# Performance work log

Hardware: AMD Instinct MI355X
Metric: run time of the kernel (lower is better)

Reference implementation:

```python
import jax, jax.numpy as jnp
import numpy as np

N = 100000      # num nodes
E = 1600000     # num edges (before self-loops)
F_IN = 500      # num_features
H1, C1 = 8, 8   # heads, hidden_dim (layer 1, concat)
H2, C2 = 1, 16  # output_heads, num_classes (layer 2, mean)
NEG_SLOPE = 0.2


def setup_inputs() -> dict:
    key = jax.random.key(0)
    ks = jax.random.split(key, 10)
    x = jax.random.normal(ks[0], (N, F_IN), dtype=jnp.float32)
    edge_index = jax.random.randint(ks[1], (2, E), 0, N, dtype=jnp.int64)
    s = 0.05
    W1 = jax.random.normal(ks[2], (F_IN, H1 * C1), dtype=jnp.float32) * s
    a_src1 = jax.random.normal(ks[3], (H1, C1), dtype=jnp.float32) * s
    a_dst1 = jax.random.normal(ks[4], (H1, C1), dtype=jnp.float32) * s
    b1 = jnp.zeros((H1 * C1,), dtype=jnp.float32)
    W2 = jax.random.normal(ks[5], (H1 * C1, H2 * C2), dtype=jnp.float32) * s
    a_src2 = jax.random.normal(ks[6], (H2, C2), dtype=jnp.float32) * s
    a_dst2 = jax.random.normal(ks[7], (H2, C2), dtype=jnp.float32) * s
    b2 = jnp.zeros((C2,), dtype=jnp.float32)
    return {"x": x, "edge_index": edge_index, "W1": W1, "a_src1": a_src1,
            "a_dst1": a_dst1, "b1": b1, "W2": W2, "a_src2": a_src2,
            "a_dst2": a_dst2, "b2": b2}


def _gat_conv(x, src, dst, W, a_src, a_dst, bias, heads, out_c, concat):
    n = x.shape[0]
    xw = (x @ W).reshape(n, heads, out_c)                      # [N,H,C]
    # per-node attention halves, gathered per edge -> logits [E,H]
    s_src = jnp.einsum('nhc,hc->nh', xw, a_src)
    s_dst = jnp.einsum('nhc,hc->nh', xw, a_dst)
    e = s_src[src] + s_dst[dst]
    e = jnp.where(e > 0, e, NEG_SLOPE * e)                     # leaky_relu
    # segment softmax over incoming edges of each target node
    m = jax.ops.segment_max(e, dst, num_segments=n)            # [N,H]
    m = jnp.where(jnp.isfinite(m), m, 0.0)
    p = jnp.exp(e - m[dst])                                    # [E,H]
    denom = jax.ops.segment_sum(p, dst, num_segments=n)        # [N,H]
    alpha = p / denom[dst]                                     # [E,H]
    # scatter-aggregate weighted messages
    out = jax.ops.segment_sum(alpha[:, :, None] * xw[src], dst,
                              num_segments=n)                  # [N,H,C]
    if concat:
        out = out.reshape(n, heads * out_c)
    else:
        out = out.mean(axis=1)
    return out + bias


def reference(x, edge_index, W1, a_src1, a_dst1, b1, W2, a_src2, a_dst2, b2):
    # PyG GATConv adds self-loops by default
    loops = jnp.arange(N, dtype=edge_index.dtype)
    src = jnp.concatenate([edge_index[0], loops])
    dst = jnp.concatenate([edge_index[1], loops])
    # eval mode: dropout is identity
    h = _gat_conv(x, src, dst, W1, a_src1, a_dst1, b1, H1, C1, True)
    h = jax.nn.elu(h)
    h = _gat_conv(h, src, dst, W2, a_src2, a_dst2, b2, H2, C2, False)
    return jax.nn.log_softmax(h, axis=1)
```

## Files before the change

kernel.cpp:

```cpp
#include <hip/hip_runtime.h>
#include <hip/hip_bf16.h>
#include <math.h>

#define NEGS 0.2f
#define BSH 9
#define TS 4096

typedef __attribute__((ext_vector_type(8))) short bf16x8;
typedef __attribute__((ext_vector_type(8))) unsigned short u16x8;
typedef __attribute__((ext_vector_type(4))) float f32x4;

__device__ __forceinline__ unsigned short f2bf(float f) {
  __hip_bfloat16 h = __float2bfloat16(f);
  unsigned short u;
  __builtin_memcpy(&u, &h, 2);
  return u;
}
__device__ __forceinline__ float bf2f(unsigned short u) {
  return __uint_as_float((unsigned)u << 16);
}
__device__ __forceinline__ unsigned packbf(float lo, float hi) {
  return (unsigned)f2bf(lo) | ((unsigned)f2bf(hi) << 16);
}


__device__ __forceinline__ void dev_wcvt(const float* __restrict__ W1,
                                         unsigned short* __restrict__ Wb,
                                         int K, int Kp, int blk) {
  int t = blk * 256 + threadIdx.x;
  if (t >= Kp * 64) return;
  int kg = t >> 6, c = t & 63;
  float f = (kg < K) ? W1[(size_t)kg * 64 + c] : 0.f;
  size_t off = ((size_t)((kg >> 5) * 4 + ((kg >> 3) & 3)) * 512) + c * 8 + (kg & 7);
  Wb[off] = f2bf(f);
}

__device__ __forceinline__ void dev_thist(const int* __restrict__ ei,
                                          int* __restrict__ hist,
                                          int E, int NB, int tile) {
  __shared__ int lh[256];
  const int t = threadIdx.x;
  lh[t] = 0;
  __syncthreads();
  const int e0 = tile * TS;
#pragma unroll
  for (int j = 0; j < TS / 256; ++j) {
    int e = e0 + j * 256 + t;
    if (e < E) atomicAdd(&lh[ei[E + e] >> BSH], 1);
  }
  __syncthreads();
  if (t < NB) hist[tile * NB + t] = lh[t];
}

__device__ __forceinline__ void dev_bscan1(const int* __restrict__ hist,
                                           int* __restrict__ off_rel,
                                           int* __restrict__ total,
                                           int NT, int NB, int b) {
  __shared__ int sh[256];
  const int t = threadIdx.x;
  int t0 = 2 * t, t1 = 2 * t + 1;
  int v0 = (t0 < NT) ? hist[t0 * NB + b] : 0;
  int v1 = (t1 < NT) ? hist[t1 * NB + b] : 0;
  int ps = v0 + v1;
  sh[t] = ps;
  __syncthreads();
  for (int off = 1; off < 256; off <<= 1) {
    int v = (t >= off) ? sh[t - off] : 0;
    __syncthreads();
    sh[t] += v;
    __syncthreads();
  }
  int excl = sh[t] - ps;
  if (t0 < NT) off_rel[t0 * NB + b] = excl;
  if (t1 < NT) off_rel[t1 * NB + b] = excl + v0;
  if (t == 255) total[b] = sh[255];
}

__device__ __forceinline__ void dev_pscatter(const int* __restrict__ ei,
                                             const int* __restrict__ off_rel,
                                             const int* __restrict__ total,
                                             unsigned* __restrict__ pairs,
                                             int E, int NB, int tile) {
  __shared__ int cur[256];
  __shared__ int sb[256];
  const int t = threadIdx.x;
  int v = (t < NB) ? total[t] : 0;
  sb[t] = v;
  __syncthreads();
  for (int off = 1; off < 256; off <<= 1) {
    int x = (t >= off) ? sb[t - off] : 0;
    __syncthreads();
    sb[t] += x;
    __syncthreads();
  }
  if (t < NB) cur[t] = (sb[t] - v) + off_rel[tile * NB + t];
  __syncthreads();
  const int e0 = tile * TS;
#pragma unroll
  for (int j = 0; j < TS / 256; ++j) {
    int e = e0 + j * 256 + t;
    if (e < E) {
      int s = ei[e], d = ei[E + e];
      int pos = atomicAdd(&cur[d >> BSH], 1);
      pairs[pos] = ((unsigned)(d & ((1 << BSH) - 1)) << 23) | (unsigned)s;
    }
  }
}

__device__ __forceinline__ void dev_bcsr(const unsigned* __restrict__ pairs,
                                         const int* __restrict__ total,
                                         int* __restrict__ rowptr,
                                         int* __restrict__ col,
                                         int Nn, int E, int NB, int b) {
  __shared__ int cnt[1 << BSH];
  __shared__ int cu[1 << BSH];
  __shared__ int sh[256];
  __shared__ int P0, P1;
  const int t = threadIdx.x;
  const int d0 = b << BSH;
  const int dn = min(1 << BSH, Nn - d0);
  {
    int v = (t < NB) ? total[t] : 0;
    sh[t] = v;
    __syncthreads();
    for (int off = 1; off < 256; off <<= 1) {
      int x = (t >= off) ? sh[t - off] : 0;
      __syncthreads();
      sh[t] += x;
      __syncthreads();
    }
    if (t == b) { P0 = sh[t] - v; P1 = sh[t]; }
    __syncthreads();
  }
  const int p0 = P0, p1 = P1;
  const int rpb = p0 + d0;
  cnt[2 * t] = (2 * t < dn) ? 1 : 0;
  cnt[2 * t + 1] = (2 * t + 1 < dn) ? 1 : 0;
  __syncthreads();
  for (int i = p0 + t; i < p1; i += 256) atomicAdd(&cnt[pairs[i] >> 23], 1);
  __syncthreads();
  int a0 = cnt[2 * t], a1 = cnt[2 * t + 1];
  int ps = a0 + a1;
  sh[t] = ps;
  __syncthreads();
  for (int off = 1; off < 256; off <<= 1) {
    int v = (t >= off) ? sh[t - off] : 0;
    __syncthreads();
    sh[t] += v;
    __syncthreads();
  }
  int excl = sh[t] - ps;
#pragma unroll
  for (int u = 0; u < 2; ++u) {
    int i = 2 * t + u;
    int ex = (u == 0) ? excl : excl + a0;
    if (i < dn) {
      rowptr[d0 + i] = rpb + ex;
      col[rpb + ex] = d0 + i;
      cu[i] = ex + 1;
    }
  }
  if (b == NB - 1 && t == 0) rowptr[Nn] = E + Nn;
  __syncthreads();
  for (int i = p0 + t; i < p1; i += 256) {
    unsigned p = pairs[i];
    int pos = atomicAdd(&cu[p >> 23], 1);
    col[rpb + pos] = (int)(p & 0x7fffffu);
  }
}

__device__ __forceinline__ void dev_gemm(const float* __restrict__ A,
                                         const unsigned short* __restrict__ Wb,
                                         unsigned short* __restrict__ C,
                                         const float* __restrict__ a1s,
                                         const float* __restrict__ a1d,
                                         float* __restrict__ ssrc,
                                         float* __restrict__ sdst,
                                         int M, int K, int nck, int rowblk) {
  const int tid = threadIdx.x;
  const int lane = tid & 63;
  const int w = tid >> 6;
  const int r15 = lane & 15;
  const int kgrp = lane >> 4;
  const int bm = rowblk * 64;
  const int row = bm + w * 16 + r15;
  const float* Ar = A + (size_t)(row < M ? row : (M - 1)) * K;

  f32x4 acc[4] = {};

  for (int ck = 0; ck < nck; ++ck) {
#pragma unroll
    for (int ks = 0; ks < 2; ++ks) {
      const int k0 = ck * 64 + ks * 32 + kgrp * 8;
      bf16x8 af;
      if (ck < nck - 1) {
        const float4* g = (const float4*)(Ar + k0);
        float4 f0 = g[0], f1 = g[1];
        unsigned pk[4] = { packbf(f0.x, f0.y), packbf(f0.z, f0.w),
                           packbf(f1.x, f1.y), packbf(f1.z, f1.w) };
        af = *(bf16x8*)pk;
      } else {
        float f[8];
#pragma unroll
        for (int j = 0; j < 8; ++j) {
          int kk = k0 + j;
          f[j] = (kk < K) ? Ar[kk] : 0.f;
        }
        unsigned pk[4];
#pragma unroll
        for (int j = 0; j < 4; ++j) pk[j] = packbf(f[2 * j], f[2 * j + 1]);
        af = *(bf16x8*)pk;
      }
      const unsigned short* bb =
          Wb + ((size_t)((ck * 2 + ks) * 4 + kgrp) * 512) + r15 * 8;
      bf16x8 bf4[4];
#pragma unroll
      for (int nc = 0; nc < 4; ++nc)
        bf4[nc] = *(const bf16x8*)(bb + nc * 128);
#pragma unroll
      for (int nc = 0; nc < 4; ++nc)
        acc[nc] = __builtin_amdgcn_mfma_f32_16x16x32_bf16(af, bf4[nc], acc[nc], 0, 0, 0);
    }
  }
  float av[4], dv[4];
#pragma unroll
  for (int nc = 0; nc < 4; ++nc) {
    av[nc] = a1s[nc * 16 + r15];
    dv[nc] = a1d[nc * 16 + r15];
  }
#pragma unroll
  for (int j = 0; j < 4; ++j) {
    int grow = bm + w * 16 + kgrp * 4 + j;
    bool liv = grow < M;
#pragma unroll
    for (int nc = 0; nc < 4; ++nc) {
      if (liv) C[(size_t)grow * 64 + nc * 16 + r15] = f2bf(acc[nc][j]);
      float ss = acc[nc][j] * av[nc];
      float sd = acc[nc][j] * dv[nc];
      ss += __shfl_xor(ss, 1); ss += __shfl_xor(ss, 2); ss += __shfl_xor(ss, 4);
      sd += __shfl_xor(sd, 1); sd += __shfl_xor(sd, 2); sd += __shfl_xor(sd, 4);
      if ((r15 & 7) == 0 && liv) {
        int h = nc * 2 + (r15 >> 3);
        ssrc[grow * 8 + h] = ss;
        sdst[grow * 8 + h] = sd;
      }
    }
  }
}

__global__ __launch_bounds__(256) void k_A(const float* __restrict__ W1,
                                           unsigned short* __restrict__ Wb,
                                           int K, int Kp,
                                           const int* __restrict__ ei,
                                           int* __restrict__ hist,
                                           int E, int NB, int WCB) {
  int b = blockIdx.x;
  if (b < WCB) dev_wcvt(W1, Wb, K, Kp, b);
  else dev_thist(ei, hist, E, NB, b - WCB);
}

__global__ __launch_bounds__(256) void k_B1(const int* __restrict__ hist,
                                            int* __restrict__ off_rel,
                                            int* __restrict__ total,
                                            int NT, int NB,
                                            const float* __restrict__ A,
                                            const unsigned short* __restrict__ Wb,
                                            unsigned short* __restrict__ C,
                                            const float* __restrict__ a1s,
                                            const float* __restrict__ a1d,
                                            float* __restrict__ ssrc,
                                            float* __restrict__ sdst,
                                            int M, int K, int nck, int R0) {
  int b = blockIdx.x;
  if (b < NB) dev_bscan1(hist, off_rel, total, NT, NB, b);
  else dev_gemm(A, Wb, C, a1s, a1d, ssrc, sdst, M, K, nck, b - NB + R0);
}

__global__ __launch_bounds__(256) void k_B2(const int* __restrict__ ei,
                                            const int* __restrict__ off_rel,
                                            const int* __restrict__ total,
                                            unsigned* __restrict__ pairs,
                                            int E, int NB, int NT,
                                            const float* __restrict__ A,
                                            const unsigned short* __restrict__ Wb,
                                            unsigned short* __restrict__ C,
                                            const float* __restrict__ a1s,
                                            const float* __restrict__ a1d,
                                            float* __restrict__ ssrc,
                                            float* __restrict__ sdst,
                                            int M, int K, int nck, int R0) {
  int b = blockIdx.x;
  if (b < NT) dev_pscatter(ei, off_rel, total, pairs, E, NB, b);
  else dev_gemm(A, Wb, C, a1s, a1d, ssrc, sdst, M, K, nck, b - NT + R0);
}

__global__ __launch_bounds__(256) void k_B3(const unsigned* __restrict__ pairs,
                                            const int* __restrict__ total,
                                            int* __restrict__ rowptr,
                                            int* __restrict__ col,
                                            int Nn, int E, int NB,
                                            const float* __restrict__ A,
                                            const unsigned short* __restrict__ Wb,
                                            unsigned short* __restrict__ C,
                                            const float* __restrict__ a1s,
                                            const float* __restrict__ a1d,
                                            float* __restrict__ ssrc,
                                            float* __restrict__ sdst,
                                            int M, int K, int nck, int R0) {
  int b = blockIdx.x;
  if (b < NB) dev_bcsr(pairs, total, rowptr, col, Nn, E, NB, b);
  else dev_gemm(A, Wb, C, a1s, a1d, ssrc, sdst, M, K, nck, b - NB + R0);
}

__global__ __launch_bounds__(256) void k_agg1(const int* __restrict__ rowptr,
                                              const int* __restrict__ col,
                                              const float* __restrict__ ssrc,
                                              const float* __restrict__ sdst,
                                              const unsigned short* __restrict__ xwb,
                                              const float* __restrict__ b1,
                                              float* __restrict__ h1, int Nn) {
  int wid = (blockIdx.x * 256 + threadIdx.x) >> 6;
  if (wid >= Nn) return;
  int lane = threadIdx.x & 63;
  int slot = lane >> 3;
  int chg = lane & 7;
  float sd = sdst[wid * 8 + chg];
  int start = rowptr[wid], end = rowptr[wid + 1];
  float den = 0.f;
  float acc[8] = {};
  for (int it = start; it < end; it += 8) {
    int idx = it + slot;
    bool ok = idx < end;
    int s = col[ok ? idx : start];
    u16x8 pv = *(const u16x8*)(xwb + (size_t)s * 64 + chg * 8);
    float v = ssrc[s * 8 + chg] + sd;
    v = v > 0.f ? v : NEGS * v;
    float p = ok ? __expf(v) : 0.f;
    den += p;
#pragma unroll
    for (int j = 0; j < 8; ++j) acc[j] = fmaf(p, bf2f(pv[j]), acc[j]);
  }
#pragma unroll
  for (int off = 8; off < 64; off <<= 1) {
    den += __shfl_xor(den, off);
#pragma unroll
    for (int j = 0; j < 8; ++j) acc[j] += __shfl_xor(acc[j], off);
  }
  if (slot == 0) {
    float inv = 1.f / den;
    float o[8];
#pragma unroll
    for (int j = 0; j < 8; ++j) {
      float v = acc[j] * inv + b1[chg * 8 + j];
      o[j] = v > 0.f ? v : (__expf(v) - 1.f);
    }
    float* dst = h1 + (size_t)wid * 64 + chg * 8;
#pragma unroll
    for (int j = 0; j < 8; ++j) dst[j] = o[j];
  }
}

__global__ __launch_bounds__(256) void k_gemm2p(const float* __restrict__ h1,
                                                const float* __restrict__ W2,
                                                const float* __restrict__ asr,
                                                const float* __restrict__ adt,
                                                unsigned short* __restrict__ xw2b,
                                                float* __restrict__ ssrc,
                                                float* __restrict__ sdst, int Nn) {
  __shared__ float w[64 * 16];
  int tid = threadIdx.x;
  for (int i = tid; i < 1024; i += 256) w[i] = W2[i];
  __syncthreads();
  int idx = blockIdx.x * 256 + tid;
  if (idx >= Nn * 16) return;
  int n = idx >> 4, c = idx & 15;
  const float* hr = h1 + (size_t)n * 64;
  float acc = 0.f;
#pragma unroll 8
  for (int k = 0; k < 64; ++k) acc += hr[k] * w[k * 16 + c];
  xw2b[idx] = f2bf(acc);
  float ssv = acc * asr[c], sdv = acc * adt[c];
#pragma unroll
  for (int off = 1; off < 16; off <<= 1) {
    ssv += __shfl_xor(ssv, off);
    sdv += __shfl_xor(sdv, off);
  }
  if (c == 0) { ssrc[n] = ssv; sdst[n] = sdv; }
}

__global__ __launch_bounds__(256) void k_agg2(const int* __restrict__ rowptr,
                                              const int* __restrict__ col,
                                              const float* __restrict__ ssrc,
                                              const float* __restrict__ sdst,
                                              const unsigned short* __restrict__ xw2b,
                                              const float* __restrict__ b2,
                                              float* __restrict__ out, int Nn) {
  int wid = (blockIdx.x * 256 + threadIdx.x) >> 6;
  if (wid >= Nn) return;
  int lane = threadIdx.x & 63;
  int slot = lane >> 4, c = lane & 15;
  float sd = sdst[wid];
  int start = rowptr[wid], end = rowptr[wid + 1];
  float den = 0.f, acc = 0.f;
  int i = start + slot;
  for (; i + 4 < end; i += 8) {
    int s0 = col[i], s1 = col[i + 4];
    float w0 = bf2f(xw2b[(size_t)s0 * 16 + c]);
    float w1 = bf2f(xw2b[(size_t)s1 * 16 + c]);
    float v0 = ssrc[s0] + sd; v0 = v0 > 0.f ? v0 : NEGS * v0;
    float v1 = ssrc[s1] + sd; v1 = v1 > 0.f ? v1 : NEGS * v1;
    float p0 = __expf(v0), p1 = __expf(v1);
    den += p0 + p1;
    acc = fmaf(p0, w0, acc);
    acc = fmaf(p1, w1, acc);
  }
  if (i < end) {
    int s = col[i];
    float v = ssrc[s] + sd;
    v = v > 0.f ? v : NEGS * v;
    float p = __expf(v);
    den += p;
    acc = fmaf(p, bf2f(xw2b[(size_t)s * 16 + c]), acc);
  }
  den += __shfl_xor(den, 16);
  den += __shfl_xor(den, 32);
  acc += __shfl_xor(acc, 16);
  acc += __shfl_xor(acc, 32);
  float o = acc / den + b2[c];
  float mx = o;
#pragma unroll
  for (int off = 1; off < 16; off <<= 1) mx = fmaxf(mx, __shfl_xor(mx, off));
  float ex = __expf(o - mx);
  float ssum = ex;
#pragma unroll
  for (int off = 1; off < 16; off <<= 1) ssum += __shfl_xor(ssum, off);
  float r = o - mx - __logf(ssum);
  if (slot == 0) out[(size_t)wid * 16 + c] = r;
}

extern "C" void kernel_launch(void* const* d_in, const int* in_sizes, int n_in,
                              void* d_out, int out_size, void* d_ws, size_t ws_size,
                              hipStream_t stream) {
  const float* x      = (const float*)d_in[0];
  const int* ei       = (const int*)d_in[1];
  const float* W1     = (const float*)d_in[2];
  const float* a_src1 = (const float*)d_in[3];
  const float* a_dst1 = (const float*)d_in[4];
  const float* b1     = (const float*)d_in[5];
  const float* W2     = (const float*)d_in[6];
  const float* a_src2 = (const float*)d_in[7];
  const float* a_dst2 = (const float*)d_in[8];
  const float* b2     = (const float*)d_in[9];

  const int F    = in_sizes[2] / 64;
  const int Nn   = in_sizes[0] / F;
  const int E    = in_sizes[1] / 2;
  const int Etot = E + Nn;
  const int nck  = (F + 63) >> 6;
  const int Kp   = nck * 64;
  const int NB   = (Nn + (1 << BSH) - 1) >> BSH;
  const int NT   = (E + TS - 1) / TS;
  const int WCB  = (Kp * 64 + 255) / 256;
  const int GB   = (Nn + 63) / 64;
  const int G1   = (GB + 2) / 3;
  const int G2   = G1;
  const int G3   = GB - G1 - G2;

  float* ws = (float*)d_ws;
  unsigned short* xwb = (unsigned short*)ws;
  float* h1     = ws + (size_t)Nn * 32;
  float* ssrc1  = h1 + (size_t)Nn * 64;
  float* sdst1  = ssrc1 + (size_t)Nn * 8;
  int* rowptr   = (int*)(sdst1 + (size_t)Nn * 8);
  int* col      = rowptr + Nn + 1;
  unsigned short* Wb = (unsigned short*)(col + ((Etot + 7) & ~7));
  int* hist     = (int*)(Wb + (size_t)Kp * 64);
  int* off_rel  = hist + (size_t)NT * NB;
  int* total    = off_rel + (size_t)NT * NB;
  unsigned* pairs = (unsigned*)h1;
  unsigned short* xw2b = (unsigned short*)ws;
  float* ssrc2  = ws + (size_t)Nn * 8;
  float* sdst2  = ssrc2 + Nn;
  float* out2   = (float*)d_out;

  dim3 blk(256);

  k_A<<<dim3(WCB + NT), blk, 0, stream>>>(W1, Wb, F, Kp, ei, hist, E, NB, WCB);
  k_B1<<<dim3(NB + G1), blk, 0, stream>>>(hist, off_rel, total, NT, NB,
      x, Wb, xwb, a_src1, a_dst1, ssrc1, sdst1, Nn, F, nck, 0);
  k_B2<<<dim3(NT + G2), blk, 0, stream>>>(ei, off_rel, total, pairs, E, NB, NT,
      x, Wb, xwb, a_src1, a_dst1, ssrc1, sdst1, Nn, F, nck, G1);
  k_B3<<<dim3(NB + G3), blk, 0, stream>>>(pairs, total, rowptr, col, Nn, E, NB,
      x, Wb, xwb, a_src1, a_dst1, ssrc1, sdst1, Nn, F, nck, G1 + G2);
  k_agg1<<<dim3((Nn * 64 + 255) / 256), blk, 0, stream>>>(
      rowptr, col, ssrc1, sdst1, xwb, b1, h1, Nn);
  k_gemm2p<<<dim3((Nn * 16 + 255) / 256), blk, 0, stream>>>(
      h1, W2, a_src2, a_dst2, xw2b, ssrc2, sdst2, Nn);
  k_agg2<<<dim3((Nn * 64 + 255) / 256), blk, 0, stream>>>(
      rowptr, col, ssrc2, sdst2, xw2b, b2, out2, Nn);
}
```

Baseline: 239.4 us.

## Prefetch next A tile in layer-1 GEMM and recompute source scores in aggregation

The layer-1 GEMM loop is flattened into 32-wide k-steps, with the next iteration's fp32 A values loaded into registers while the current step's MFMAs run. This is meant to hide global-load latency. Separately, the per-node source attention score is no longer computed and stored by the GEMM. The aggregation kernel instead recomputes it per edge from the bf16 xw row it already loads, dotted with a_src. This removes the ssrc write and the per-edge ssrc gather, at the cost of extra FMAs per edge and logits computed from bf16-rounded features.

```diff
diff --git a/kernel.cpp b/kernel.cpp
--- a/kernel.cpp
+++ b/kernel.cpp
@@ -172,9 +172,7 @@
 __device__ __forceinline__ void dev_gemm(const float* __restrict__ A,
                                          const unsigned short* __restrict__ Wb,
                                          unsigned short* __restrict__ C,
-                                         const float* __restrict__ a1s,
                                          const float* __restrict__ a1d,
-                                         float* __restrict__ ssrc,
                                          float* __restrict__ sdst,
                                          int M, int K, int nck, int rowblk) {
   const int tid = threadIdx.x;
@@ -185,49 +183,50 @@
   const int bm = rowblk * 64;
   const int row = bm + w * 16 + r15;
   const float* Ar = A + (size_t)(row < M ? row : (M - 1)) * K;
+  const int NIT = 2 * nck;
+  const int ITV = (K >= 40) ? ((K - 40) / 32 + 1) : 0;
 
   f32x4 acc[4] = {};
 
-  for (int ck = 0; ck < nck; ++ck) {
-#pragma unroll
-    for (int ks = 0; ks < 2; ++ks) {
-      const int k0 = ck * 64 + ks * 32 + kgrp * 8;
-      bf16x8 af;
-      if (ck < nck - 1) {
+  float4 c0, c1;
+  {
+    const float4* g = (const float4*)(Ar + kgrp * 8);
+    c0 = g[0]; c1 = g[1];
+  }
+  for (int it = 0; it < NIT; ++it) {
+    float4 n0, n1;
+    if (it + 1 < NIT) {
+      int k0 = (it + 1) * 32 + kgrp * 8;
+      if (it + 1 < ITV) {
         const float4* g = (const float4*)(Ar + k0);
-        float4 f0 = g[0], f1 = g[1];
-        unsigned pk[4] = { packbf(f0.x, f0.y), packbf(f0.z, f0.w),
-                           packbf(f1.x, f1.y), packbf(f1.z, f1.w) };
-        af = *(bf16x8*)pk;
+        n0 = g[0]; n1 = g[1];
       } else {
-        float f[8];
+        float tmp[8];
 #pragma unroll
         for (int j = 0; j < 8; ++j) {
           int kk = k0 + j;
-          f[j] = (kk < K) ? Ar[kk] : 0.f;
+          tmp[j] = (kk < K) ? Ar[kk] : 0.f;
         }
-        unsigned pk[4];
-#pragma unroll
-        for (int j = 0; j < 4; ++j) pk[j] = packbf(f[2 * j], f[2 * j + 1]);
-        af = *(bf16x8*)pk;
+        n0 = make_float4(tmp[0], tmp[1], tmp[2], tmp[3]);
+        n1 = make_float4(tmp[4], tmp[5], tmp[6], tmp[7]);
       }
-      const unsigned short* bb =
-          Wb + ((size_t)((ck * 2 + ks) * 4 + kgrp) * 512) + r15 * 8;
-      bf16x8 bf4[4];
-#pragma unroll
-      for (int nc = 0; nc < 4; ++nc)
-        bf4[nc] = *(const bf16x8*)(bb + nc * 128);
-#pragma unroll
-      for (int nc = 0; nc < 4; ++nc)
-        acc[nc] = __builtin_amdgcn_mfma_f32_16x16x32_bf16(af, bf4[nc], acc[nc], 0, 0, 0);
-    }
-  }
-  float av[4], dv[4];
-#pragma unroll
-  for (int nc = 0; nc < 4; ++nc) {
-    av[nc] = a1s[nc * 16 + r15];
-    dv[nc] = a1d[nc * 16 + r15];
-  }
+    }
+    const unsigned short* bb = Wb + ((size_t)(it * 4 + kgrp) * 512) + r15 * 8;
+    bf16x8 bf4[4];
+#pragma unroll
+    for (int nc = 0; nc < 4; ++nc)
+      bf4[nc] = *(const bf16x8*)(bb + nc * 128);
+    unsigned pk[4] = { packbf(c0.x, c0.y), packbf(c0.z, c0.w),
+                       packbf(c1.x, c1.y), packbf(c1.z, c1.w) };
+    bf16x8 af = *(bf16x8*)pk;
+#pragma unroll
+    for (int nc = 0; nc < 4; ++nc)
+      acc[nc] = __builtin_amdgcn_mfma_f32_16x16x32_bf16(af, bf4[nc], acc[nc], 0, 0, 0);
+    c0 = n0; c1 = n1;
+  }
+  float dv[4];
+#pragma unroll
+  for (int nc = 0; nc < 4; ++nc) dv[nc] = a1d[nc * 16 + r15];
 #pragma unroll
   for (int j = 0; j < 4; ++j) {
     int grow = bm + w * 16 + kgrp * 4 + j;
@@ -235,15 +234,10 @@
 #pragma unroll
     for (int nc = 0; nc < 4; ++nc) {
       if (liv) C[(size_t)grow * 64 + nc * 16 + r15] = f2bf(acc[nc][j]);
-      float ss = acc[nc][j] * av[nc];
       float sd = acc[nc][j] * dv[nc];
-      ss += __shfl_xor(ss, 1); ss += __shfl_xor(ss, 2); ss += __shfl_xor(ss, 4);
       sd += __shfl_xor(sd, 1); sd += __shfl_xor(sd, 2); sd += __shfl_xor(sd, 4);
-      if ((r15 & 7) == 0 && liv) {
-        int h = nc * 2 + (r15 >> 3);
-        ssrc[grow * 8 + h] = ss;
-        sdst[grow * 8 + h] = sd;
-      }
+      if ((r15 & 7) == 0 && liv)
+        sdst[grow * 8 + nc * 2 + (r15 >> 3)] = sd;
     }
   }
 }
@@ -266,14 +260,12 @@
                                             const float* __restrict__ A,
                                             const unsigned short* __restrict__ Wb,
                                             unsigned short* __restrict__ C,
-                                            const float* __restrict__ a1s,
                                             const float* __restrict__ a1d,
-                                            float* __restrict__ ssrc,
                                             float* __restrict__ sdst,
                                             int M, int K, int nck, int R0) {
   int b = blockIdx.x;
   if (b < NB) dev_bscan1(hist, off_rel, total, NT, NB, b);
-  else dev_gemm(A, Wb, C, a1s, a1d, ssrc, sdst, M, K, nck, b - NB + R0);
+  else dev_gemm(A, Wb, C, a1d, sdst, M, K, nck, b - NB + R0);
 }
 
 __global__ __launch_bounds__(256) void k_B2(const int* __restrict__ ei,
@@ -284,14 +276,12 @@
                                             const float* __restrict__ A,
                                             const unsigned short* __restrict__ Wb,
                                             unsigned short* __restrict__ C,
-                                            const float* __restrict__ a1s,
                                             const float* __restrict__ a1d,
-                                            float* __restrict__ ssrc,
                                             float* __restrict__ sdst,
                                             int M, int K, int nck, int R0) {
   int b = blockIdx.x;
   if (b < NT) dev_pscatter(ei, off_rel, total, pairs, E, NB, b);
-  else dev_gemm(A, Wb, C, a1s, a1d, ssrc, sdst, M, K, nck, b - NT + R0);
+  else dev_gemm(A, Wb, C, a1d, sdst, M, K, nck, b - NT + R0);
 }
 
 __global__ __launch_bounds__(256) void k_B3(const unsigned* __restrict__ pairs,
@@ -302,19 +292,17 @@
                                             const float* __restrict__ A,
                                             const unsigned short* __restrict__ Wb,
                                             unsigned short* __restrict__ C,
-                                            const float* __restrict__ a1s,
                                             const float* __restrict__ a1d,
-                                            float* __restrict__ ssrc,
                                             float* __restrict__ sdst,
                                             int M, int K, int nck, int R0) {
   int b = blockIdx.x;
   if (b < NB) dev_bcsr(pairs, total, rowptr, col, Nn, E, NB, b);
-  else dev_gemm(A, Wb, C, a1s, a1d, ssrc, sdst, M, K, nck, b - NB + R0);
+  else dev_gemm(A, Wb, C, a1d, sdst, M, K, nck, b - NB + R0);
 }
 
 __global__ __launch_bounds__(256) void k_agg1(const int* __restrict__ rowptr,
                                               const int* __restrict__ col,
-                                              const float* __restrict__ ssrc,
+                                              const float* __restrict__ a1s,
                                               const float* __restrict__ sdst,
                                               const unsigned short* __restrict__ xwb,
                                               const float* __restrict__ b1,
@@ -324,6 +312,9 @@
   int lane = threadIdx.x & 63;
   int slot = lane >> 3;
   int chg = lane & 7;
+  float asr[8];
+#pragma unroll
+  for (int j = 0; j < 8; ++j) asr[j] = a1s[chg * 8 + j];
   float sd = sdst[wid * 8 + chg];
   int start = rowptr[wid], end = rowptr[wid + 1];
   float den = 0.f;
@@ -333,12 +324,18 @@
     bool ok = idx < end;
     int s = col[ok ? idx : start];
     u16x8 pv = *(const u16x8*)(xwb + (size_t)s * 64 + chg * 8);
-    float v = ssrc[s * 8 + chg] + sd;
+    float f[8];
+#pragma unroll
+    for (int j = 0; j < 8; ++j) f[j] = bf2f(pv[j]);
+    float ss = 0.f;
+#pragma unroll
+    for (int j = 0; j < 8; ++j) ss = fmaf(f[j], asr[j], ss);
+    float v = ss + sd;
     v = v > 0.f ? v : NEGS * v;
     float p = ok ? __expf(v) : 0.f;
     den += p;
 #pragma unroll
-    for (int j = 0; j < 8; ++j) acc[j] = fmaf(p, bf2f(pv[j]), acc[j]);
+    for (int j = 0; j < 8; ++j) acc[j] = fmaf(p, f[j], acc[j]);
   }
 #pragma unroll
   for (int off = 8; off < 64; off <<= 1) {
@@ -487,13 +484,13 @@
 
   k_A<<<dim3(WCB + NT), blk, 0, stream>>>(W1, Wb, F, Kp, ei, hist, E, NB, WCB);
   k_B1<<<dim3(NB + G1), blk, 0, stream>>>(hist, off_rel, total, NT, NB,
-      x, Wb, xwb, a_src1, a_dst1, ssrc1, sdst1, Nn, F, nck, 0);
+      x, Wb, xwb, a_dst1, sdst1, Nn, F, nck, 0);
   k_B2<<<dim3(NT + G2), blk, 0, stream>>>(ei, off_rel, total, pairs, E, NB, NT,
-      x, Wb, xwb, a_src1, a_dst1, ssrc1, sdst1, Nn, F, nck, G1);
+      x, Wb, xwb, a_dst1, sdst1, Nn, F, nck, G1);
   k_B3<<<dim3(NB + G3), blk, 0, stream>>>(pairs, total, rowptr, col, Nn, E, NB,
-      x, Wb, xwb, a_src1, a_dst1, ssrc1, sdst1, Nn, F, nck, G1 + G2);
+      x, Wb, xwb, a_dst1, sdst1, Nn, F, nck, G1 + G2);
   k_agg1<<<dim3((Nn * 64 + 255) / 256), blk, 0, stream>>>(
-      rowptr, col, ssrc1, sdst1, xwb, b1, h1, Nn);
+      rowptr, col, a_src1, sdst1, xwb, b1, h1, Nn);
   k_gemm2p<<<dim3((Nn * 16 + 255) / 256), blk, 0, stream>>>(
       h1, W2, a_src2, a_dst2, xw2b, ssrc2, sdst2, Nn);
   k_agg2<<<dim3((Nn * 64 + 255) / 256), blk, 0, stream>>>(
```

Result: faster. 220.6 us (-7.8%).
